# Optimization experiments

Measured on AMD Instinct MI355X. Metric: run time of the kernel, lower is better.

## Reference

```python
import jax, jax.numpy as jnp
import numpy as np
import math

D_MODEL = 2048
D_STATE = 64
D_CONV = 4
EXPAND = 2
HEADDIM = 128
NGROUPS = 1
CHUNK = 256
D_INNER = EXPAND * D_MODEL            # 4096
NHEADS = D_INNER // HEADDIM           # 32
CONV_DIM = D_INNER + 2 * NGROUPS * D_STATE   # 4224
D_IN_PROJ = 2 * D_INNER + 2 * NGROUPS * D_STATE + NHEADS  # 8352
BATCH, SEQLEN = 2, 4096
EPS = 1e-5


def segsum(x):
    # x: (..., T) -> (..., T, T) with s[i, j] = sum_{k=j+1}^{i} x[k], -inf above diag
    T = x.shape[-1]
    xx = jnp.broadcast_to(x[..., :, None], x.shape + (T,))
    mask_lo = jnp.tril(jnp.ones((T, T), dtype=bool), -1)
    xx = jnp.where(mask_lo, xx, 0.0)
    s = jnp.cumsum(xx, axis=-2)
    mask = jnp.tril(jnp.ones((T, T), dtype=bool), 0)
    return jnp.where(mask, s, -jnp.inf)


def ssd(X, A, B, C, block_len):
    # X:(b,L,h,p)  A:(b,L,h)  B,C:(b,L,h,n)
    b, L, h, p = X.shape
    c = L // block_len
    X = X.reshape(b, c, block_len, h, p)
    A = A.reshape(b, c, block_len, h).transpose(0, 3, 1, 2)  # b h c l
    B = B.reshape(b, c, block_len, h, -1)
    C = C.reshape(b, c, block_len, h, -1)
    A_cumsum = jnp.cumsum(A, axis=-1)
    Lmat = jnp.exp(segsum(A))                                  # b h c l l
    Y_diag = jnp.einsum('bclhn,bcshn,bhcls,bcshp->bclhp', C, B, Lmat, X)
    decay_states = jnp.exp(A_cumsum[:, :, :, -1:] - A_cumsum)  # b h c l
    states = jnp.einsum('bclhn,bhcl,bclhp->bchpn', B, decay_states, X)
    init = jnp.zeros_like(states[:, :1])
    states = jnp.concatenate([init, states], axis=1)
    decay_chunk = jnp.exp(segsum(jnp.pad(A_cumsum[:, :, :, -1], ((0, 0), (0, 0), (1, 0)))))
    new_states = jnp.einsum('bhzc,bchpn->bzhpn', decay_chunk, states)
    states, final_state = new_states[:, :-1], new_states[:, -1]
    Y_off = jnp.einsum('bclhn,bchpn,bhcl->bclhp', C, states, jnp.exp(A_cumsum))
    Y = (Y_diag + Y_off).reshape(b, L, h, p)
    return Y, final_state


def causal_dwconv(x, w, b):
    # x:(B,L,C)  w:(C,K) depthwise kernel  b:(C,)  -> causal conv, length preserved
    C, K = w.shape
    y = jax.lax.conv_general_dilated(
        x.transpose(0, 2, 1), w[:, None, :], (1,), [(K - 1, 0)],
        feature_group_count=C)
    return y.transpose(0, 2, 1) + b


def setup_inputs() -> dict:
    key = jax.random.key(0)
    ks = jax.random.split(key, 8)
    u = jax.random.normal(ks[0], (BATCH, SEQLEN, D_MODEL), dtype=jnp.float32)
    W_in = jax.random.normal(ks[1], (D_MODEL, D_IN_PROJ), dtype=jnp.float32) / np.sqrt(D_MODEL)
    conv_w = jax.random.normal(ks[2], (CONV_DIM, D_CONV), dtype=jnp.float32) / np.sqrt(D_CONV)
    conv_b = jnp.zeros((CONV_DIM,), dtype=jnp.float32)
    # dt_bias init: inverse-softplus of dt sampled log-uniform in [dt_min, dt_max]
    dt_min, dt_max, dt_floor = 1e-3, 1e-1, 1e-4
    dt = jnp.exp(jax.random.uniform(ks[3], (NHEADS,)) * (math.log(dt_max) - math.log(dt_min)) + math.log(dt_min))
    dt = jnp.clip(dt, dt_floor)
    dt_bias = dt + jnp.log(-jnp.expm1(-dt))
    A_log = jnp.log(jax.random.uniform(ks[4], (NHEADS,), minval=1.0, maxval=16.0))
    D = jnp.ones((NHEADS,), dtype=jnp.float32)
    norm_w = jnp.ones((D_INNER,), dtype=jnp.float32)
    W_out = jax.random.normal(ks[5], (D_INNER, D_MODEL), dtype=jnp.float32) / np.sqrt(D_INNER)
    return {"u": u, "W_in": W_in, "conv_w": conv_w, "conv_b": conv_b,
            "dt_bias": dt_bias, "A_log": A_log, "D": D, "norm_w": norm_w, "W_out": W_out}


def reference(u, W_in, conv_w, conv_b, dt_bias, A_log, D, norm_w, W_out):
    batch, seqlen, _ = u.shape
    zxbcdt = u @ W_in                                   # (B,L,8352)
    z, xBC, dt = jnp.split(zxbcdt, [D_INNER, D_INNER + CONV_DIM], axis=-1)
    dt = jax.nn.softplus(dt + dt_bias)                  # (B,L,H)
    xBC = jax.nn.silu(causal_dwconv(xBC, conv_w, conv_b))
    x, B, C = jnp.split(xBC, [D_INNER, D_INNER + NGROUPS * D_STATE], axis=-1)
    x = x.reshape(batch, seqlen, NHEADS, HEADDIM)
    B = jnp.broadcast_to(B.reshape(batch, seqlen, NGROUPS, D_STATE), (batch, seqlen, NHEADS, D_STATE))
    C = jnp.broadcast_to(C.reshape(batch, seqlen, NGROUPS, D_STATE), (batch, seqlen, NHEADS, D_STATE))
    A = -jnp.exp(A_log)                                 # (H,)
    x_scaled = x * dt[..., None]
    A_dt = A * dt                                       # (B,L,H)
    y, _final = ssd(x_scaled, A_dt, B, C, CHUNK)
    y = y.reshape(batch, seqlen, D_INNER)
    x_flat = x.reshape(batch, seqlen, D_INNER)
    D_full = jnp.repeat(D, HEADDIM)
    y = y + x_flat * D_full
    # gated RMSNorm, norm AFTER gate (norm_before_gate=False)
    yg = y * jax.nn.silu(z)
    var = jnp.mean(yg * yg, axis=-1, keepdims=True)
    y = yg * jax.lax.rsqrt(var + EPS) * norm_w
    return y @ W_out
```

## Files before the change

### kernel.cpp

```cpp
#include <hip/hip_runtime.h>

typedef short s8v __attribute__((ext_vector_type(8)));
typedef float f4v __attribute__((ext_vector_type(4)));
typedef unsigned short bfu;

#define MFMA16 __builtin_amdgcn_mfma_f32_16x16x32_bf16

constexpr int kSEQ = 4096;
constexpr int kBL  = 8192;
constexpr int kDM  = 2048;
constexpr int kDP  = 8352;
constexpr int kDPpad = 8448;
constexpr int kDI  = 4096;
constexpr int kCV  = 4224;
constexpr int kXBC = 4256;
constexpr int kNH  = 32;
constexpr int kHD  = 128;
constexpr int kDS  = 64;
constexpr int kCH  = 256;
constexpr int kLDW = 2112;
constexpr int kLDY = 4160;

#if defined(__has_builtin)
#  if __has_builtin(__builtin_amdgcn_global_load_lds)
#    define HAS_GLD 1
#  endif
#endif
#ifndef HAS_GLD
#  define HAS_GLD 0
#endif

__device__ __forceinline__ void gld_lds16(const void* g, void* lbase, int lane){
#if HAS_GLD
  (void)lane;
  __builtin_amdgcn_global_load_lds(
      (const __attribute__((address_space(1))) void*)g,
      (__attribute__((address_space(3))) void*)lbase, 16, 0, 0);
#else
  *(uint4*)((char*)lbase + lane * 16) = *(const uint4*)g;
#endif
}

__device__ __forceinline__ bfu f2bf(float f){
  union { float f; unsigned u; } c; c.f = f;
  return (bfu)((c.u + 0x7fffu + ((c.u >> 16) & 1u)) >> 16);
}
__device__ __forceinline__ float bf2f(bfu s){
  union { unsigned u; float f; } c; c.u = ((unsigned)s) << 16;
  return c.f;
}

__device__ __forceinline__ s8v frag_ld(const char* lds, int rowbase, int kh, int lane){
  int r = rowbase + (lane & 15);
  int slot = (kh << 2) + (lane >> 4);
  return *(const s8v*)(lds + (((r << 3) + (slot ^ (r & 7))) << 4));
}

__global__ __launch_bounds__(256) void k_zero(bfu* __restrict__ p, int n){
  int i = blockIdx.x * 256 + threadIdx.x;
  if (i < n) p[i] = 0;
}

__global__ __launch_bounds__(256) void k_cvt(const float* __restrict__ s, bfu* __restrict__ d, int n8){
  int i = blockIdx.x * 256 + threadIdx.x;
  int stride = gridDim.x * 256;
  for (; i < n8; i += stride){
    const float4* sp = (const float4*)(s + (size_t)i * 8);
    float4 a = sp[0], b = sp[1];
    uint4 pk; bfu* pp = (bfu*)&pk;
    pp[0]=f2bf(a.x); pp[1]=f2bf(a.y); pp[2]=f2bf(a.z); pp[3]=f2bf(a.w);
    pp[4]=f2bf(b.x); pp[5]=f2bf(b.y); pp[6]=f2bf(b.z); pp[7]=f2bf(b.w);
    *(uint4*)(d + (size_t)i * 8) = pk;
  }
}

__global__ __launch_bounds__(256) void k_transpose(const float* __restrict__ src, bfu* __restrict__ dst,
                                                   int R, int C, const float* __restrict__ scale, int ldo){
  __shared__ float tile[32][33];
  int c0 = blockIdx.x * 32, r0 = blockIdx.y * 32;
  int tx = threadIdx.x, ty = threadIdx.y;
  #pragma unroll
  for (int i = ty; i < 32; i += 8){
    int r = r0 + i, cc = c0 + tx;
    tile[i][tx] = (r < R && cc < C) ? src[(size_t)r * C + cc] : 0.f;
  }
  __syncthreads();
  #pragma unroll
  for (int i = ty; i < 32; i += 8){
    int dr = c0 + i, dc = r0 + tx;
    if (dr < C && dc < R){
      float v = tile[tx][i];
      if (scale) v *= scale[dc];
      dst[(size_t)dr * ldo + dc] = f2bf(v);
    }
  }
}

template<int MODE>
__global__ __launch_bounds__(512, 2) void k_gemm256(const bfu* __restrict__ A, const bfu* __restrict__ Bt,
                                                    float* __restrict__ outF, bfu* __restrict__ outZ,
                                                    bfu* __restrict__ outX, const float* __restrict__ rsv,
                                                    int tilesN, int N, int K, int lda, int ldb){
  extern __shared__ char lds[];
  int t = threadIdx.x, lane = t & 63, wave = t >> 6;
  int wr = wave >> 2, wc = wave & 3;
  int nwg = gridDim.x;
  int bid = blockIdx.x;
  int cpx = nwg >> 3;
  int wg = (bid & 7) * cpx + (bid >> 3);
  int bandSz = tilesN << 2;
  int band = wg / bandSz;
  int rem  = wg - band * bandSz;
  int tnTile = rem >> 2;
  int tmTile = (band << 2) + (rem & 3);
  int tm = tmTile << 8, tn = tnTile << 8;
  const bfu* Ab = A + (size_t)tm * lda;
  const bfu* Bb = Bt + (size_t)tn * ldb;

  #define AU(b,kh) ((b) * 65536 + (kh) * 16384)
  #define BU(b,kh) ((b) * 65536 + 32768 + (kh) * 16384)

  auto stage_unit = [&](const bfu* srcbase, int ld, int unitOfs, int kcol0){
    #pragma unroll
    for (int j = 0; j < 2; ++j){
      int lg = j * 512 + wave * 64 + lane;
      int r = lg >> 2;
      int s = (lg & 3) ^ ((r >> 1) & 3);
      gld_lds16(srcbase + (size_t)r * ld + kcol0 + s * 8,
                lds + unitOfs + (j * 512 + wave * 64) * 16, lane);
    }
  };
  auto rd_frag = [&](int unitOfs, int rbase) -> s8v {
    int r = rbase + (lane & 15);
    int s = lane >> 4;
    int g = (r << 2) + (s ^ ((r >> 1) & 3));
    return *(const s8v*)(lds + unitOfs + (g << 4));
  };

  f4v acc[8][4];
  f4v zz = {0.f, 0.f, 0.f, 0.f};
  #pragma unroll
  for (int m = 0; m < 8; ++m)
    #pragma unroll
    for (int n = 0; n < 4; ++n) acc[m][n] = zz;

  int nt = K >> 6;
  stage_unit(Ab, lda, AU(0,0), 0);
  stage_unit(Bb, ldb, BU(0,0), 0);
  stage_unit(Ab, lda, AU(0,1), 32);
  stage_unit(Bb, ldb, BU(0,1), 32);
  __builtin_amdgcn_sched_barrier(0);
  asm volatile("s_waitcnt vmcnt(4)" ::: "memory");
  __builtin_amdgcn_sched_barrier(0);
  __builtin_amdgcn_s_barrier();
  __builtin_amdgcn_sched_barrier(0);

  #pragma unroll 1
  for (int tt = 0; tt < nt; ++tt){
    int cb = tt & 1, nb = cb ^ 1;
    int k0n = (tt + 1) << 6;
    bool more = (tt + 1 < nt);
    #pragma unroll
    for (int kh = 0; kh < 2; ++kh){
      if (more){
        stage_unit(Ab, lda, AU(nb,kh), k0n + kh * 32);
        stage_unit(Bb, ldb, BU(nb,kh), k0n + kh * 32);
      }
      s8v af[8], bf[4];
      #pragma unroll
      for (int m = 0; m < 8; ++m) af[m] = rd_frag(AU(cb,kh), wr * 128 + m * 16);
      #pragma unroll
      for (int n = 0; n < 4; ++n) bf[n] = rd_frag(BU(cb,kh), wc * 64 + n * 16);
      __builtin_amdgcn_s_setprio(1);
      #pragma unroll
      for (int n = 0; n < 4; ++n)
        #pragma unroll
        for (int m = 0; m < 8; ++m)
          acc[m][n] = MFMA16(af[m], bf[n], acc[m][n], 0, 0, 0);
      __builtin_amdgcn_s_setprio(0);
      __builtin_amdgcn_sched_barrier(0);
      if (more) { asm volatile("s_waitcnt vmcnt(4)" ::: "memory"); }
      else      { asm volatile("s_waitcnt vmcnt(0)" ::: "memory"); }
      __builtin_amdgcn_sched_barrier(0);
      __builtin_amdgcn_s_barrier();
      __builtin_amdgcn_sched_barrier(0);
    }
  }

  int r0 = (lane >> 4) << 2;
  if (MODE == 0){
    float* rsl = (float*)lds;
    if (t < 256) rsl[t] = rsv[tm + t];
    __syncthreads();
    #pragma unroll
    for (int m = 0; m < 8; ++m)
      #pragma unroll
      for (int n = 0; n < 4; ++n)
        #pragma unroll
        for (int r = 0; r < 4; ++r){
          int rl = wr * 128 + m * 16 + r0 + r;
          size_t rg = (size_t)(tm + rl);
          int cg = tn + wc * 64 + n * 16 + (lane & 15);
          outF[rg * N + cg] = acc[m][n][r] * rsl[rl];
        }
  } else {
    #pragma unroll
    for (int m = 0; m < 8; ++m)
      #pragma unroll
      for (int n = 0; n < 4; ++n){
        int col = wc * 64 + n * 16 + (lane & 15);
        int cs = col >> 3, cl = col & 7;
        #pragma unroll
        for (int r = 0; r < 4; ++r){
          int row = wr * 128 + m * 16 + r0 + r;
          *(bfu*)(lds + row * 512 + ((cs ^ (row & 7)) << 4) + cl * 2) = f2bf(acc[m][n][r]);
        }
      }
    __syncthreads();
    bfu* op; int ldo, cofs;
    if (tn < 4096){ op = outZ; ldo = 4096; cofs = 0; }
    else          { op = outX; ldo = kXBC; cofs = 4096; }
    int row = t >> 1, half = t & 1;
    bfu* baseo = op + (size_t)(tm + row) * ldo + (tn - cofs) + half * 128;
    #pragma unroll
    for (int i = 0; i < 16; ++i){
      int cg = tn + half * 128 + i * 8;
      if (cg < kDP){
        uint4 v = *(const uint4*)(lds + row * 512 + (((half * 16 + i) ^ (row & 7)) << 4));
        *(uint4*)(baseo + i * 8) = v;
      }
    }
  }
  #undef AU
  #undef BU
}

__global__ __launch_bounds__(256) void k_conv(const bfu* __restrict__ xbc, const float* __restrict__ cw,
    const float* __restrict__ cb, bfu* __restrict__ xT,
    bfu* __restrict__ B16o, bfu* __restrict__ BTo, bfu* __restrict__ C16o){
  int cht = blockIdx.x;
  int lt = blockIdx.y;
  int b = lt >> 6;
  int l0 = (lt & 63) << 6;
  int t = threadIdx.x;
  __shared__ float w[256];
  __shared__ float bias[64];
  __shared__ bfu in16[67][66];
  __shared__ bfu out16[64][66];
  if (t < 64) bias[t] = cb[cht * 64 + t];
  w[t] = cw[cht * 256 + t];
  int chbase = cht * 64;
  for (int i = t; i < 67 * 64; i += 256){
    int rrow = i >> 6, cc = i & 63;
    int l = l0 + rrow - 3;
    bfu hv = 0;
    if (l >= 0) hv = xbc[((size_t)b * kSEQ + l) * kXBC + chbase + cc];
    in16[rrow][cc] = hv;
  }
  __syncthreads();
  for (int i = t; i < 4096; i += 256){
    int lr = i >> 6, cc = i & 63;
    float acc = bias[cc];
    #pragma unroll
    for (int j = 0; j < 4; ++j)
      acc += bf2f(in16[lr + j][cc]) * w[cc * 4 + j];
    float sv = acc / (1.f + __expf(-acc));
    out16[lr][cc] = f2bf(sv);
  }
  __syncthreads();
  if (chbase >= 4096){
    for (int i = t; i < 4096; i += 256){
      int lr = i >> 6, cc = i & 63;
      size_t row = (size_t)b * kSEQ + l0 + lr;
      int ch = chbase + cc;
      bfu v = out16[lr][cc];
      if (ch < 4096 + kDS) B16o[row * kDS + (ch - 4096)] = v;
      else                 C16o[row * kDS + (ch - 4096 - kDS)] = v;
    }
  }
  if (chbase < 4096 + kDS){
    for (int i = t; i < 4096; i += 256){
      int cc = i >> 6, lr = i & 63;
      int ch = chbase + cc;
      int lg = l0 + lr;
      bfu v = out16[lr][cc];
      if (ch < 4096){
        int hh = ch >> 7, p = ch & 127;
        xT[(((size_t)b * kNH + hh) * kHD + p) * kSEQ + lg] = v;
      } else if (ch < 4096 + kDS){
        BTo[((size_t)b * kDS + (ch - 4096)) * kSEQ + lg] = v;
      }
    }
  }
}

__global__ __launch_bounds__(256) void k_dtscan(const bfu* __restrict__ xbc, const float* __restrict__ dt_bias,
    const float* __restrict__ A_log, float* __restrict__ dtf, float* __restrict__ acum){
  int bi = blockIdx.x;
  int h = bi & 31, c = (bi >> 5) & 15, b = bi >> 9;
  int t = threadIdx.x;
  size_t row = (size_t)b * kSEQ + c * kCH + t;
  float draw = bf2f(xbc[row * kXBC + kCV + h]) + dt_bias[h];
  float dt = (draw > 20.f) ? draw : log1pf(__expf(draw));
  dtf[row * kNH + h] = dt;
  float dA = -__expf(A_log[h]) * dt;
  __shared__ float s[256];
  s[t] = dA;
  __syncthreads();
  #pragma unroll
  for (int off = 1; off < 256; off <<= 1){
    float v = (t >= off) ? s[t - off] : 0.f;
    __syncthreads();
    s[t] += v;
    __syncthreads();
  }
  acum[(size_t)bi * 256 + t] = s[t];
}

__global__ __launch_bounds__(256) void k_states(const bfu* __restrict__ xT, const bfu* __restrict__ BT,
    const float* __restrict__ dtf, const float* __restrict__ acum, bfu* __restrict__ states){
  int bi = blockIdx.x;
  int h = bi & 31, c = (bi >> 5) & 15, b = bi >> 9;
  int t = threadIdx.x, lane = t & 63, wave = t >> 6;
  int wr = wave >> 1, wc = wave & 1;
  __shared__ uint4 ldsX4[1024];
  __shared__ uint4 ldsB4[512];
  __shared__ float dsv[256];
  char* ldsX = (char*)ldsX4;
  char* ldsB = (char*)ldsB4;
  float Atot = acum[(size_t)bi * 256 + 255];
  {
    size_t row = (size_t)b * kSEQ + c * kCH + t;
    dsv[t] = dtf[row * kNH + h] * __expf(Atot - acum[(size_t)bi * 256 + t]);
  }
  f4v zz = {0.f, 0.f, 0.f, 0.f};
  f4v acc[4][2];
  #pragma unroll
  for (int m = 0; m < 4; ++m){ acc[m][0] = zz; acc[m][1] = zz; }
  const bfu* xTp = xT + ((size_t)b * kNH + h) * kHD * kSEQ + c * kCH;
  const bfu* BTp = BT + (size_t)b * kDS * kSEQ + c * kCH;
  __syncthreads();
  for (int kb = 0; kb < 4; ++kb){
    #pragma unroll
    for (int it = 0; it < 4; ++it){
      int s = it * 256 + t;
      int row = s >> 3;
      int srcslot = (s & 7) ^ (row & 7);
      gld_lds16(xTp + (size_t)row * kSEQ + kb * 64 + srcslot * 8,
                ldsX + it * 4096 + wave * 1024, lane);
    }
    #pragma unroll
    for (int it = 0; it < 2; ++it){
      int cidx = it * 256 + t;
      int row = cidx >> 3, slot = cidx & 7;
      uint4 v = *(const uint4*)(BTp + (size_t)row * kSEQ + kb * 64 + slot * 8);
      bfu* hp = (bfu*)&v;
      #pragma unroll
      for (int j = 0; j < 8; ++j)
        hp[j] = f2bf(bf2f(hp[j]) * dsv[kb * 64 + slot * 8 + j]);
      *(uint4*)(ldsB + (((row << 3) + (slot ^ (row & 7))) << 4)) = v;
    }
    __syncthreads();
    s8v af[4][2], bb[2][2];
    #pragma unroll
    for (int m = 0; m < 4; ++m){
      af[m][0] = frag_ld(ldsX, wr * 64 + m * 16, 0, lane);
      af[m][1] = frag_ld(ldsX, wr * 64 + m * 16, 1, lane);
    }
    #pragma unroll
    for (int nf = 0; nf < 2; ++nf){
      bb[nf][0] = frag_ld(ldsB, wc * 32 + nf * 16, 0, lane);
      bb[nf][1] = frag_ld(ldsB, wc * 32 + nf * 16, 1, lane);
    }
    #pragma unroll
    for (int kh = 0; kh < 2; ++kh)
      #pragma unroll
      for (int m = 0; m < 4; ++m)
        #pragma unroll
        for (int nf = 0; nf < 2; ++nf)
          acc[m][nf] = MFMA16(af[m][kh], bb[nf][kh], acc[m][nf], 0, 0, 0);
    __syncthreads();
  }
  bfu* sp = states + (size_t)bi * 8192;
  int r0 = (lane >> 4) << 2;
  #pragma unroll
  for (int m = 0; m < 4; ++m)
    #pragma unroll
    for (int nf = 0; nf < 2; ++nf)
      #pragma unroll
      for (int r = 0; r < 4; ++r){
        int p = wr * 64 + m * 16 + r0 + r;
        int n = wc * 32 + nf * 16 + (lane & 15);
        sp[p * 64 + n] = f2bf(acc[m][nf][r]);
      }
}

__global__ __launch_bounds__(256) void k_scan(bfu* __restrict__ st, const float* __restrict__ acum){
  int bh = blockIdx.x >> 2;
  int jg = blockIdx.x & 3;
  int b = bh >> 5, h = bh & 31;
  int t = threadIdx.x;
  float run[8];
  #pragma unroll
  for (int j = 0; j < 8; ++j) run[j] = 0.f;
  for (int c = 0; c < 16; ++c){
    size_t bi = (size_t)((b * 16 + c) * 32 + h);
    float eT = __expf(acum[bi * 256 + 255]);
    size_t base = bi * 8192 + (size_t)jg * 2048;
    #pragma unroll
    for (int j = 0; j < 8; ++j){
      size_t idx = base + j * 256 + t;
      float sl = bf2f(st[idx]);
      st[idx] = f2bf(run[j]);
      run[j] = run[j] * eT + sl;
    }
  }
}

__global__ __launch_bounds__(256) void k_y(
    const bfu* __restrict__ xT, const bfu* __restrict__ Bm, const bfu* __restrict__ Cm,
    const bfu* __restrict__ SIs, const float* __restrict__ dtf, const float* __restrict__ acum,
    const bfu* __restrict__ z16, const float* __restrict__ Dp,
    bfu* __restrict__ y16)
{
  int bi = blockIdx.x;
  int h = bi & 31, c = (bi >> 5) & 15, b = bi >> 9;
  int ph = blockIdx.y;
  int t = threadIdx.x, lane = t & 63, wave = t >> 6;
  int wl = wave << 6;
  __shared__ uint4 ldsP4[2048];
  __shared__ uint4 ldsT4[512];
  __shared__ float acumS[256];
  __shared__ float dtS[256];
  char* ldsP = ((char*)ldsP4) + (wave << 13);
  char* ldsT = (char*)ldsT4;
  size_t rowbase = (size_t)b * kSEQ + c * kCH;
  acumS[t] = acum[(size_t)bi * 256 + t];
  dtS[t] = dtf[(rowbase + t) * kNH + h];
  const bfu* SIp = SIs + (size_t)bi * 8192 + (size_t)ph * 4096;
  #pragma unroll
  for (int it = 0; it < 2; ++it){
    int cidx = it * 256 + t;
    int row = cidx >> 3, slot = cidx & 7;
    uint4 v = *(const uint4*)(SIp + row * 64 + slot * 8);
    *(uint4*)(ldsT + (((row << 3) + (slot ^ (row & 7))) << 4)) = v;
  }
  const bfu* Cp = Cm + rowbase * kDS;
  s8v cf[4][2];
  #pragma unroll
  for (int m = 0; m < 4; ++m){
    cf[m][0] = *(const s8v*)(Cp + (size_t)(wl + m * 16 + (lane & 15)) * kDS + ((lane >> 4) << 3));
    cf[m][1] = *(const s8v*)(Cp + (size_t)(wl + m * 16 + (lane & 15)) * kDS + 32 + ((lane >> 4) << 3));
  }
  __syncthreads();
  float Arow[16];
  #pragma unroll
  for (int m = 0; m < 4; ++m)
    #pragma unroll
    for (int r = 0; r < 4; ++r)
      Arow[m * 4 + r] = acumS[wl + m * 16 + ((lane >> 4) << 2) + r];
  f4v acc[4][4];
  {
    s8v bfo[4][2];
    #pragma unroll
    for (int pf = 0; pf < 4; ++pf){
      bfo[pf][0] = frag_ld(ldsT, pf << 4, 0, lane);
      bfo[pf][1] = frag_ld(ldsT, pf << 4, 1, lane);
    }
    f4v zz = {0.f, 0.f, 0.f, 0.f};
    #pragma unroll
    for (int m = 0; m < 4; ++m)
      #pragma unroll
      for (int pf = 0; pf < 4; ++pf){
        f4v v = zz;
        v = MFMA16(cf[m][0], bfo[pf][0], v, 0, 0, 0);
        v = MFMA16(cf[m][1], bfo[pf][1], v, 0, 0, 0);
        #pragma unroll
        for (int r = 0; r < 4; ++r) v[r] *= __expf(Arow[m * 4 + r]);
        acc[m][pf] = v;
      }
  }
  float Dh = Dp[h];
  const bfu* Bp = Bm + rowbase * kDS;
  const bfu* xTp = xT + (((size_t)b * kNH + h) * kHD + ph * 64) * kSEQ + c * kCH;
  #pragma unroll 1
  for (int sb = 0; sb < 4; ++sb){
    __syncthreads();
    #pragma unroll
    for (int it = 0; it < 2; ++it){
      int s = it * 256 + t;
      int row = s >> 3;
      int srcslot = (s & 7) ^ (row & 7);
      gld_lds16(xTp + (size_t)row * kSEQ + sb * 64 + srcslot * 8,
                ldsT + it * 4096 + wave * 1024, lane);
    }
    f4v sv[4][4];
    {
      s8v bsf[4][2];
      #pragma unroll
      for (int sf = 0; sf < 4; ++sf){
        bsf[sf][0] = *(const s8v*)(Bp + (size_t)(sb * 64 + sf * 16 + (lane & 15)) * kDS + ((lane >> 4) << 3));
        bsf[sf][1] = *(const s8v*)(Bp + (size_t)(sb * 64 + sf * 16 + (lane & 15)) * kDS + 32 + ((lane >> 4) << 3));
      }
      f4v zz = {0.f, 0.f, 0.f, 0.f};
      #pragma unroll
      for (int m = 0; m < 4; ++m)
        #pragma unroll
        for (int sf = 0; sf < 4; ++sf){
          f4v v = zz;
          v = MFMA16(cf[m][0], bsf[sf][0], v, 0, 0, 0);
          v = MFMA16(cf[m][1], bsf[sf][1], v, 0, 0, 0);
          sv[m][sf] = v;
        }
    }
    int scb = sb << 6;
    float As[4], dts_[4];
    #pragma unroll
    for (int sf = 0; sf < 4; ++sf){
      As[sf] = acumS[scb + sf * 16 + (lane & 15)];
      dts_[sf] = dtS[scb + sf * 16 + (lane & 15)];
    }
    #pragma unroll
    for (int m = 0; m < 4; ++m)
      #pragma unroll
      for (int sf = 0; sf < 4; ++sf)
        #pragma unroll
        for (int r = 0; r < 4; ++r){
          int rloc = m * 16 + ((lane >> 4) << 2) + r;
          int scl = sf * 16 + (lane & 15);
          int d = (wl + rloc) - (scb + scl);
          float pv = 0.f;
          if (d >= 0)
            pv = sv[m][sf][r] * __expf(Arow[m * 4 + r] - As[sf]) * dts_[sf];
          if (d == 0)
            pv += Dh;
          *(bfu*)(ldsP + rloc * 128 + ((((scl >> 3) ^ (rloc & 7)) << 3) + (scl & 7)) * 2) = f2bf(pv);
        }
    __syncthreads();
    s8v xb[4][2];
    #pragma unroll
    for (int pf = 0; pf < 4; ++pf){
      xb[pf][0] = frag_ld(ldsT, pf << 4, 0, lane);
      xb[pf][1] = frag_ld(ldsT, pf << 4, 1, lane);
    }
    #pragma unroll
    for (int m = 0; m < 4; ++m){
      s8v pa0 = frag_ld(ldsP, m << 4, 0, lane);
      s8v pa1 = frag_ld(ldsP, m << 4, 1, lane);
      #pragma unroll
      for (int pf = 0; pf < 4; ++pf){
        acc[m][pf] = MFMA16(pa0, xb[pf][0], acc[m][pf], 0, 0, 0);
        acc[m][pf] = MFMA16(pa1, xb[pf][1], acc[m][pf], 0, 0, 0);
      }
    }
  }
  __syncthreads();
  char* ldsY = (char*)ldsP4;
  #pragma unroll
  for (int m = 0; m < 4; ++m)
    #pragma unroll
    for (int pf = 0; pf < 4; ++pf)
      #pragma unroll
      for (int r = 0; r < 4; ++r){
        int rloc = wl + m * 16 + ((lane >> 4) << 2) + r;
        int col  = (pf << 4) + (lane & 15);
        *(bfu*)(ldsY + rloc * 128 + (((col >> 3) ^ (rloc & 7)) << 4) + (col & 7) * 2) = f2bf(acc[m][pf][r]);
      }
  __syncthreads();
  int cg0 = (h << 7) + (ph << 6);
  #pragma unroll
  for (int j = 0; j < 8; ++j){
    int idx = j * 256 + t;
    int row = idx >> 3, g = idx & 7;
    uint4 yv = *(const uint4*)(ldsY + row * 128 + ((g ^ (row & 7)) << 4));
    size_t rowg = rowbase + row;
    uint4 zv4 = *(const uint4*)(z16 + rowg * kDI + cg0 + g * 8);
    const bfu* yp = (const bfu*)&yv;
    const bfu* zp = (const bfu*)&zv4;
    uint4 out; bfu* op = (bfu*)&out;
    #pragma unroll
    for (int e = 0; e < 8; ++e){
      float zv = bf2f(zp[e]);
      float sg = zv / (1.f + __expf(-zv));
      op[e] = f2bf(bf2f(yp[e]) * sg);
    }
    *(uint4*)(y16 + rowg * kLDY + cg0 + g * 8) = out;
  }
}

__global__ __launch_bounds__(256) void k_rms(const bfu* __restrict__ y, float* __restrict__ rs){
  int row = blockIdx.x;
  int t = threadIdx.x, lane = t & 63, wave = t >> 6;
  const bfu* yp = y + (size_t)row * kLDY;
  uint4 a = *(const uint4*)(yp + t * 8);
  uint4 b = *(const uint4*)(yp + 2048 + t * 8);
  const bfu* ap = (const bfu*)&a;
  const bfu* bp = (const bfu*)&b;
  float ss = 0.f;
  #pragma unroll
  for (int j = 0; j < 8; ++j){
    float va = bf2f(ap[j]); ss += va * va;
    float vb = bf2f(bp[j]); ss += vb * vb;
  }
  #pragma unroll
  for (int o = 32; o > 0; o >>= 1) ss += __shfl_down(ss, o, 64);
  __shared__ float red[4];
  if (lane == 0) red[wave] = ss;
  __syncthreads();
  if (t == 0){
    float tot = red[0] + red[1] + red[2] + red[3];
    rs[row] = rsqrtf(tot * (1.f / 4096.f) + 1e-5f);
  }
}

extern "C" void kernel_launch(void* const* d_in, const int* in_sizes, int n_in,
                              void* d_out, int out_size, void* d_ws, size_t ws_size,
                              hipStream_t stream){
  (void)in_sizes; (void)n_in; (void)out_size; (void)ws_size;
  const float* u       = (const float*)d_in[0];
  const float* W_in    = (const float*)d_in[1];
  const float* conv_w  = (const float*)d_in[2];
  const float* conv_b  = (const float*)d_in[3];
  const float* dt_bias = (const float*)d_in[4];
  const float* A_log   = (const float*)d_in[5];
  const float* Dp      = (const float*)d_in[6];
  const float* norm_w  = (const float*)d_in[7];
  const float* W_out   = (const float*)d_in[8];
  char* ws = (char*)d_ws;

  const size_t o_z    = 0;
  const size_t o_xbc  = o_z   + (size_t)kBL * kDI * 2;
  const size_t o_u16  = o_xbc + (size_t)kBL * kXBC * 2;
  const size_t o_xT   = o_u16 + (size_t)kBL * kDM * 2;
  const size_t o_B16  = o_xT  + (size_t)kBL * kDI * 2;
  const size_t o_BT   = o_B16 + (size_t)kBL * kDS * 2;
  const size_t o_C16  = o_BT  + (size_t)kBL * kDS * 2;
  const size_t o_dtf  = o_C16 + (size_t)kBL * kDS * 2;
  const size_t o_acum = o_dtf + (size_t)kBL * kNH * 4;
  const size_t o_rs   = o_acum + (size_t)1024 * 256 * 4;
  const size_t o_states = o_u16;
  const size_t o_woutT  = o_u16 + (size_t)1024 * 8192 * 2;
  const size_t o_winT   = o_xT;
  const size_t o_y16    = o_xbc;

  bfu* z16    = (bfu*)(ws + o_z);
  bfu* xbc    = (bfu*)(ws + o_xbc);
  bfu* u16    = (bfu*)(ws + o_u16);
  bfu* xT     = (bfu*)(ws + o_xT);
  bfu* B16    = (bfu*)(ws + o_B16);
  bfu* BT     = (bfu*)(ws + o_BT);
  bfu* C16    = (bfu*)(ws + o_C16);
  float* dtf  = (float*)(ws + o_dtf);
  float* acum = (float*)(ws + o_acum);
  float* rs   = (float*)(ws + o_rs);
  bfu* statesS= (bfu*)(ws + o_states);
  bfu* woutT  = (bfu*)(ws + o_woutT);
  bfu* winT   = (bfu*)(ws + o_winT);
  bfu* y16    = (bfu*)(ws + o_y16);

  (void)hipFuncSetAttribute(reinterpret_cast<const void*>(&k_gemm256<2>),
                            hipFuncAttributeMaxDynamicSharedMemorySize, 131072);
  (void)hipFuncSetAttribute(reinterpret_cast<const void*>(&k_gemm256<0>),
                            hipFuncAttributeMaxDynamicSharedMemorySize, 131072);

  k_zero<<<(96 * kLDW + 255) / 256, 256, 0, stream>>>(winT + (size_t)kDP * kLDW, 96 * kLDW);
  k_cvt<<<2048, 256, 0, stream>>>(u, u16, kBL * kDM / 8);
  k_transpose<<<dim3(kDP / 32, kDM / 32), dim3(32, 8), 0, stream>>>(W_in, winT, kDM, kDP, nullptr, kLDW);
  k_gemm256<2><<<(kDPpad / 256) * (kBL / 256), 512, 131072, stream>>>(u16, winT, nullptr, z16, xbc, nullptr, kDPpad / 256, kDPpad, kDM, kDM, kLDW);
  k_conv<<<dim3(kCV / 64, kBL / 64), 256, 0, stream>>>(xbc, conv_w, conv_b, xT, B16, BT, C16);
  k_dtscan<<<1024, 256, 0, stream>>>(xbc, dt_bias, A_log, dtf, acum);
  k_transpose<<<dim3(kDM / 32, kDI / 32), dim3(32, 8), 0, stream>>>(W_out, woutT, kDI, kDM, norm_w, kDI);
  k_states<<<1024, 256, 0, stream>>>(xT, BT, dtf, acum, statesS);
  k_scan<<<256, 256, 0, stream>>>(statesS, acum);
  k_y<<<dim3(1024, 2), 256, 0, stream>>>(xT, B16, C16, statesS, dtf, acum, z16, Dp, y16);
  k_rms<<<kBL, 256, 0, stream>>>(y16, rs);
  k_gemm256<0><<<(kDM / 256) * (kBL / 256), 512, 131072, stream>>>(y16, woutT, (float*)d_out, nullptr, nullptr, rs, kDM / 256, kDM, kDI, kLDY, kDI);
}
```

Measured before the change: 851.0 us.

## Shrink GEMM tiles to 256x128 with K=32 steps for higher occupancy

Both projection GEMMs move from 256x256 output tiles with K=64 double-buffered stages to 256x128 tiles with K=32 stages. This cuts LDS from 128KB to 48KB and raises launch bounds to 4 blocks per CU. Each wave now computes a 64x64 sub-tile arranged 4x2, and the bf16 epilogue writes through LDS in two halves. The aim is more resident waves and more workgroups to hide latency. In exchange, operand reuse per loaded byte is lower, and a barrier with a full vmcnt(0) wait on every K step shortens the overlap between loads and MFMA work.

```diff
diff --git a/kernel.cpp b/kernel.cpp
--- a/kernel.cpp
+++ b/kernel.cpp
@@ -97,13 +97,13 @@
 }
 
 template<int MODE>
-__global__ __launch_bounds__(512, 2) void k_gemm256(const bfu* __restrict__ A, const bfu* __restrict__ Bt,
+__global__ __launch_bounds__(512, 4) void k_gemm256(const bfu* __restrict__ A, const bfu* __restrict__ Bt,
                                                     float* __restrict__ outF, bfu* __restrict__ outZ,
                                                     bfu* __restrict__ outX, const float* __restrict__ rsv,
                                                     int tilesN, int N, int K, int lda, int ldb){
   extern __shared__ char lds[];
   int t = threadIdx.x, lane = t & 63, wave = t >> 6;
-  int wr = wave >> 2, wc = wave & 3;
+  int wr = wave >> 1, wc = wave & 1;
   int nwg = gridDim.x;
   int bid = blockIdx.x;
   int cpx = nwg >> 3;
@@ -113,78 +113,64 @@
   int rem  = wg - band * bandSz;
   int tnTile = rem >> 2;
   int tmTile = (band << 2) + (rem & 3);
-  int tm = tmTile << 8, tn = tnTile << 8;
+  int tm = tmTile << 8, tn = tnTile << 7;
   const bfu* Ab = A + (size_t)tm * lda;
   const bfu* Bb = Bt + (size_t)tn * ldb;
 
-  #define AU(b,kh) ((b) * 65536 + (kh) * 16384)
-  #define BU(b,kh) ((b) * 65536 + 32768 + (kh) * 16384)
-
-  auto stage_unit = [&](const bfu* srcbase, int ld, int unitOfs, int kcol0){
-    #pragma unroll
-    for (int j = 0; j < 2; ++j){
-      int lg = j * 512 + wave * 64 + lane;
-      int r = lg >> 2;
-      int s = (lg & 3) ^ ((r >> 1) & 3);
-      gld_lds16(srcbase + (size_t)r * ld + kcol0 + s * 8,
-                lds + unitOfs + (j * 512 + wave * 64) * 16, lane);
-    }
+  int sr = t >> 2, scc = (t & 3) ^ ((t >> 3) & 3);
+  auto stage_half = [&](const bfu* src, int ld, int ldsOfs, int kcol0){
+    gld_lds16(src + (size_t)sr * ld + kcol0 + scc * 8,
+              lds + ldsOfs + (wave << 10), lane);
   };
-  auto rd_frag = [&](int unitOfs, int rbase) -> s8v {
-    int r = rbase + (lane & 15);
-    int s = lane >> 4;
-    int g = (r << 2) + (s ^ ((r >> 1) & 3));
-    return *(const s8v*)(lds + unitOfs + (g << 4));
-  };
-
-  f4v acc[8][4];
+  int swz = ((lane >> 4) ^ ((lane >> 1) & 3)) << 4;
+
+  f4v acc[4][4];
   f4v zz = {0.f, 0.f, 0.f, 0.f};
   #pragma unroll
-  for (int m = 0; m < 8; ++m)
+  for (int m = 0; m < 4; ++m)
     #pragma unroll
     for (int n = 0; n < 4; ++n) acc[m][n] = zz;
 
-  int nt = K >> 6;
-  stage_unit(Ab, lda, AU(0,0), 0);
-  stage_unit(Bb, ldb, BU(0,0), 0);
-  stage_unit(Ab, lda, AU(0,1), 32);
-  stage_unit(Bb, ldb, BU(0,1), 32);
+  int nt = K >> 5;
+  stage_half(Ab, lda, 0, 0);
+  stage_half(Ab + (size_t)128 * lda, lda, 8192, 0);
+  stage_half(Bb, ldb, 16384, 0);
   __builtin_amdgcn_sched_barrier(0);
-  asm volatile("s_waitcnt vmcnt(4)" ::: "memory");
+  asm volatile("s_waitcnt vmcnt(0)" ::: "memory");
   __builtin_amdgcn_sched_barrier(0);
   __builtin_amdgcn_s_barrier();
   __builtin_amdgcn_sched_barrier(0);
 
   #pragma unroll 1
   for (int tt = 0; tt < nt; ++tt){
-    int cb = tt & 1, nb = cb ^ 1;
-    int k0n = (tt + 1) << 6;
+    int cb = (tt & 1) * 24576;
     bool more = (tt + 1 < nt);
-    #pragma unroll
-    for (int kh = 0; kh < 2; ++kh){
-      if (more){
-        stage_unit(Ab, lda, AU(nb,kh), k0n + kh * 32);
-        stage_unit(Bb, ldb, BU(nb,kh), k0n + kh * 32);
-      }
-      s8v af[8], bf[4];
-      #pragma unroll
-      for (int m = 0; m < 8; ++m) af[m] = rd_frag(AU(cb,kh), wr * 128 + m * 16);
-      #pragma unroll
-      for (int n = 0; n < 4; ++n) bf[n] = rd_frag(BU(cb,kh), wc * 64 + n * 16);
-      __builtin_amdgcn_s_setprio(1);
-      #pragma unroll
-      for (int n = 0; n < 4; ++n)
-        #pragma unroll
-        for (int m = 0; m < 8; ++m)
-          acc[m][n] = MFMA16(af[m], bf[n], acc[m][n], 0, 0, 0);
-      __builtin_amdgcn_s_setprio(0);
-      __builtin_amdgcn_sched_barrier(0);
-      if (more) { asm volatile("s_waitcnt vmcnt(4)" ::: "memory"); }
-      else      { asm volatile("s_waitcnt vmcnt(0)" ::: "memory"); }
-      __builtin_amdgcn_sched_barrier(0);
-      __builtin_amdgcn_s_barrier();
-      __builtin_amdgcn_sched_barrier(0);
-    }
+    if (more){
+      int nb = ((tt + 1) & 1) * 24576;
+      int kc = (tt + 1) << 5;
+      stage_half(Ab, lda, nb, kc);
+      stage_half(Ab + (size_t)128 * lda, lda, nb + 8192, kc);
+      stage_half(Bb, ldb, nb + 16384, kc);
+    }
+    s8v af[4], bf[4];
+    #pragma unroll
+    for (int m = 0; m < 4; ++m)
+      af[m] = *(const s8v*)(lds + cb + ((wr * 64 + m * 16 + (lane & 15)) << 6) + swz);
+    #pragma unroll
+    for (int n = 0; n < 4; ++n)
+      bf[n] = *(const s8v*)(lds + cb + 16384 + ((wc * 64 + n * 16 + (lane & 15)) << 6) + swz);
+    __builtin_amdgcn_s_setprio(1);
+    #pragma unroll
+    for (int n = 0; n < 4; ++n)
+      #pragma unroll
+      for (int m = 0; m < 4; ++m)
+        acc[m][n] = MFMA16(af[m], bf[n], acc[m][n], 0, 0, 0);
+    __builtin_amdgcn_s_setprio(0);
+    __builtin_amdgcn_sched_barrier(0);
+    asm volatile("s_waitcnt vmcnt(0)" ::: "memory");
+    __builtin_amdgcn_sched_barrier(0);
+    __builtin_amdgcn_s_barrier();
+    __builtin_amdgcn_sched_barrier(0);
   }
 
   int r0 = (lane >> 4) << 2;
@@ -193,46 +179,51 @@
     if (t < 256) rsl[t] = rsv[tm + t];
     __syncthreads();
     #pragma unroll
-    for (int m = 0; m < 8; ++m)
+    for (int m = 0; m < 4; ++m)
       #pragma unroll
       for (int n = 0; n < 4; ++n)
         #pragma unroll
         for (int r = 0; r < 4; ++r){
-          int rl = wr * 128 + m * 16 + r0 + r;
+          int rl = wr * 64 + m * 16 + r0 + r;
           size_t rg = (size_t)(tm + rl);
           int cg = tn + wc * 64 + n * 16 + (lane & 15);
           outF[rg * N + cg] = acc[m][n][r] * rsl[rl];
         }
   } else {
-    #pragma unroll
-    for (int m = 0; m < 8; ++m)
-      #pragma unroll
-      for (int n = 0; n < 4; ++n){
-        int col = wc * 64 + n * 16 + (lane & 15);
-        int cs = col >> 3, cl = col & 7;
-        #pragma unroll
-        for (int r = 0; r < 4; ++r){
-          int row = wr * 128 + m * 16 + r0 + r;
-          *(bfu*)(lds + row * 512 + ((cs ^ (row & 7)) << 4) + cl * 2) = f2bf(acc[m][n][r]);
-        }
-      }
-    __syncthreads();
     bfu* op; int ldo, cofs;
     if (tn < 4096){ op = outZ; ldo = 4096; cofs = 0; }
     else          { op = outX; ldo = kXBC; cofs = 4096; }
-    int row = t >> 1, half = t & 1;
-    bfu* baseo = op + (size_t)(tm + row) * ldo + (tn - cofs) + half * 128;
-    #pragma unroll
-    for (int i = 0; i < 16; ++i){
-      int cg = tn + half * 128 + i * 8;
-      if (cg < kDP){
-        uint4 v = *(const uint4*)(lds + row * 512 + (((half * 16 + i) ^ (row & 7)) << 4));
-        *(uint4*)(baseo + i * 8) = v;
-      }
-    }
-  }
-  #undef AU
-  #undef BU
+    #pragma unroll
+    for (int h = 0; h < 2; ++h){
+      __syncthreads();
+      if ((wr >> 1) == h){
+        #pragma unroll
+        for (int m = 0; m < 4; ++m)
+          #pragma unroll
+          for (int n = 0; n < 4; ++n){
+            int col = wc * 64 + n * 16 + (lane & 15);
+            int cs = col >> 3, cl = col & 7;
+            #pragma unroll
+            for (int r = 0; r < 4; ++r){
+              int row = (wr & 1) * 64 + m * 16 + r0 + r;
+              *(bfu*)(lds + row * 256 + ((cs ^ (row & 7)) << 4) + cl * 2) = f2bf(acc[m][n][r]);
+            }
+          }
+      }
+      __syncthreads();
+      int row = t >> 2;
+      bfu* baseo = op + (size_t)(tm + h * 128 + row) * ldo + (tn - cofs);
+      #pragma unroll
+      for (int i = 0; i < 4; ++i){
+        int g = (t & 3) * 4 + i;
+        int cg = tn + g * 8;
+        if (cg < kDP){
+          uint4 v = *(const uint4*)(lds + row * 256 + ((g ^ (row & 7)) << 4));
+          *(uint4*)(baseo + g * 8) = v;
+        }
+      }
+    }
+  }
 }
 
 __global__ __launch_bounds__(256) void k_conv(const bfu* __restrict__ xbc, const float* __restrict__ cw,
@@ -659,14 +650,14 @@
   bfu* y16    = (bfu*)(ws + o_y16);
 
   (void)hipFuncSetAttribute(reinterpret_cast<const void*>(&k_gemm256<2>),
-                            hipFuncAttributeMaxDynamicSharedMemorySize, 131072);
+                            hipFuncAttributeMaxDynamicSharedMemorySize, 49152);
   (void)hipFuncSetAttribute(reinterpret_cast<const void*>(&k_gemm256<0>),
-                            hipFuncAttributeMaxDynamicSharedMemorySize, 131072);
+                            hipFuncAttributeMaxDynamicSharedMemorySize, 49152);
 
   k_zero<<<(96 * kLDW + 255) / 256, 256, 0, stream>>>(winT + (size_t)kDP * kLDW, 96 * kLDW);
   k_cvt<<<2048, 256, 0, stream>>>(u, u16, kBL * kDM / 8);
   k_transpose<<<dim3(kDP / 32, kDM / 32), dim3(32, 8), 0, stream>>>(W_in, winT, kDM, kDP, nullptr, kLDW);
-  k_gemm256<2><<<(kDPpad / 256) * (kBL / 256), 512, 131072, stream>>>(u16, winT, nullptr, z16, xbc, nullptr, kDPpad / 256, kDPpad, kDM, kDM, kLDW);
+  k_gemm256<2><<<(kDPpad / 128) * (kBL / 256), 512, 49152, stream>>>(u16, winT, nullptr, z16, xbc, nullptr, kDPpad / 128, kDPpad, kDM, kDM, kLDW);
   k_conv<<<dim3(kCV / 64, kBL / 64), 256, 0, stream>>>(xbc, conv_w, conv_b, xT, B16, BT, C16);
   k_dtscan<<<1024, 256, 0, stream>>>(xbc, dt_bias, A_log, dtf, acum);
   k_transpose<<<dim3(kDM / 32, kDI / 32), dim3(32, 8), 0, stream>>>(W_out, woutT, kDI, kDM, norm_w, kDI);
@@ -674,5 +665,5 @@
   k_scan<<<256, 256, 0, stream>>>(statesS, acum);
   k_y<<<dim3(1024, 2), 256, 0, stream>>>(xT, B16, C16, statesS, dtf, acum, z16, Dp, y16);
   k_rms<<<kBL, 256, 0, stream>>>(y16, rs);
-  k_gemm256<0><<<(kDM / 256) * (kBL / 256), 512, 131072, stream>>>(y16, woutT, (float*)d_out, nullptr, nullptr, rs, kDM / 256, kDM, kDI, kLDY, kDI);
-}
+  k_gemm256<0><<<(kDM / 128) * (kBL / 256), 512, 49152, stream>>>(y16, woutT, (float*)d_out, nullptr, nullptr, rs, kDM / 128, kDM, kDI, kLDY, kDI);
+}
```

After: 851.8 us. About the same (+0.1%).
